# Kernel tuning notes

Measured on AMD Instinct MI355X. Metric: run time of the kernel, lower is better.

Reference implementation:

```python
import jax, jax.numpy as jnp
import numpy as np
from jax.scipy.special import logsumexp

B = 2048       # anchors
P = 4          # positives per anchor (constant -> ragged list collapses to [B,P])
D = 256        # embed dim
N_NEG = 32768  # shared negative bank
TEMPERATURE = 0.05
ALPHA = 0.1
EPS = 1e-12    # F.normalize eps


def _l2norm(x):
    n = jnp.sqrt(jnp.sum(x * x, axis=-1, keepdims=True))
    return x / jnp.maximum(n, EPS)


def setup_inputs() -> dict:
    key = jax.random.key(0)
    k1, k2, k3 = jax.random.split(key, 3)
    return {
        "anchor_embeddings": jax.random.normal(k1, (B, D), jnp.float32),
        "positive_embeddings": jax.random.normal(k2, (B * P, D), jnp.float32),
        "negative_embeddings": jax.random.normal(k3, (N_NEG, D), jnp.float32),
        "num_positives_per_anchor": jnp.full((B,), P, dtype=jnp.int32),
    }


def reference(anchor_embeddings, positive_embeddings, negative_embeddings,
              num_positives_per_anchor):
    a = _l2norm(anchor_embeddings)                       # [B, D]
    p = _l2norm(positive_embeddings).reshape(B, P, D)    # [B, P, D]
    n = _l2norm(negative_embeddings)                     # [N, D]

    pos_sim = jnp.einsum("bd,bpd->bp", a, p) / TEMPERATURE   # [B, P]
    neg_sim = jnp.einsum("bd,nd->bn", a, n) / TEMPERATURE    # [B, N]  (dominant traffic)
    neg_lse = logsumexp(neg_sim, axis=1)                     # [B]

    # per-(anchor, positive) CE with label 0 over logits [pos_j, neg_sim_i]:
    # loss = logsumexp([pos_j, neg...]) - pos_j = logaddexp(pos_j, neg_lse_i) - pos_j
    pair_loss = jnp.logaddexp(pos_sim, neg_lse[:, None]) - pos_sim   # [B, P]
    counts = num_positives_per_anchor
    pair_mask = jnp.arange(P)[None, :] < counts[:, None]             # [B, P]
    total = jnp.sum(jnp.where(pair_mask, pair_loss, 0.0))

    # weighted-positive term (only for anchors with num_pos > 1)
    w = jax.nn.softmax(pos_sim, axis=1)                  # [B, P]
    wps = jnp.sum(w * pos_sim, axis=1)                   # [B]
    wloss = jnp.logaddexp(wps, neg_lse) - wps            # [B]
    total = total + ALPHA * jnp.sum(jnp.where(counts > 1, wloss, 0.0))

    return total / B
```

## Files before the change

kernel.cpp:

```cpp
#include <hip/hip_runtime.h>
#include <math.h>

constexpr int   B       = 2048;
constexpr int   P       = 4;
constexpr int   D       = 256;
constexpr int   NNEG    = 32768;
constexpr int   NTILES  = NNEG / 64;
constexpr float TEMP    = 0.05f;
constexpr float ALPHA   = 0.1f;
constexpr float EPS     = 1e-12f;
constexpr float INV_T   = 1.0f / TEMP;
constexpr float SCALE_Q = 28.853900817779268f;

typedef __bf16 bf16x8 __attribute__((ext_vector_type(8)));
typedef float  f32x4  __attribute__((ext_vector_type(4)));

__device__ inline unsigned short f2bf(float f) {
  unsigned int u = __float_as_uint(f);
  u = (u + 0x7fffu + ((u >> 16) & 1u)) >> 16;
  return (unsigned short)u;
}


__global__ void prep_kernel(const float* __restrict__ a,
                            const float* __restrict__ pzx,
                            const float* __restrict__ n,
                            unsigned short* __restrict__ a_bf,
                            unsigned short* __restrict__ n_bf,
                            float* __restrict__ pos_sim,
                            float* __restrict__ loss_acc,
                            unsigned int* __restrict__ ticket) {
  if (blockIdx.x == 0 && threadIdx.x == 0) { *loss_acc = 0.0f; *ticket = 0u; }
  int w    = (blockIdx.x * blockDim.x + threadIdx.x) >> 6;
  int lane = threadIdx.x & 63;
  if (w < B + NNEG) {
    const float* src; unsigned short* dstm; int row; float post;
    if (w < B) { src = a + (size_t)w * D;       dstm = a_bf; row = w;     post = SCALE_Q; }
    else       { src = n + (size_t)(w - B) * D; dstm = n_bf; row = w - B; post = 1.0f; }
    float4 v = ((const float4*)src)[lane];
    float ss = v.x * v.x + v.y * v.y + v.z * v.z + v.w * v.w;
#pragma unroll
    for (int off = 32; off > 0; off >>= 1) ss += __shfl_xor(ss, off, 64);
    float inv = post / fmaxf(sqrtf(ss), EPS);
    ushort4 o;
    o.x = f2bf(v.x * inv); o.y = f2bf(v.y * inv);
    o.z = f2bf(v.z * inv); o.w = f2bf(v.w * inv);
    const int p = row >> 4, r = row & 15;
    const int c = lane >> 3, q = (lane >> 1) & 3, j0 = (lane & 1) * 4;
    *(ushort4*)(dstm + (size_t)p * 4096 + c * 512 + q * 128 + r * 8 + j0) = o;
  } else {
    int pw = w - (B + NNEG);
    if (pw >= B * P) return;
    int b = pw >> 2;
    float4 av = ((const float4*)(a + (size_t)b * D))[lane];
    float4 pv = ((const float4*)(pzx + (size_t)pw * D))[lane];
    float d  = av.x * pv.x + av.y * pv.y + av.z * pv.z + av.w * pv.w;
    float sa = av.x * av.x + av.y * av.y + av.z * av.z + av.w * av.w;
    float sp = pv.x * pv.x + pv.y * pv.y + pv.z * pv.z + pv.w * pv.w;
#pragma unroll
    for (int off = 32; off > 0; off >>= 1) {
      d  += __shfl_xor(d, off, 64);
      sa += __shfl_xor(sa, off, 64);
      sp += __shfl_xor(sp, off, 64);
    }
    if (lane == 0) {
      float inva = 1.0f / fmaxf(sqrtf(sa), EPS);
      float invp = 1.0f / fmaxf(sqrtf(sp), EPS);
      pos_sim[pw] = d * inva * invp * INV_T;
    }
  }
}

constexpr int BM = 64, BN = 256;

__global__ __launch_bounds__(256, 4) void negsim_mfma_kernel(
    const unsigned short* __restrict__ Af,
    const unsigned short* __restrict__ Nf,
    float* __restrict__ part_s) {
  __shared__ __align__(16) unsigned short As[32 * 512];

  const int tid  = threadIdx.x;
  const int wave = tid >> 6;
  const int lane = tid & 63;

  const int id   = blockIdx.x;
  const int xcd  = id & 7;
  const int j    = id >> 3;
  const int nblk = xcd * 16 + (j & 15);
  const int mblk = j >> 4;
  const int m0   = mblk * BM;
  const int n0   = nblk * BN;

#pragma unroll
  for (int t = 0; t < 8; t++) {
    const int f = wave * 8 + t;
    const int c = f >> 2, p = f & 3;
    __builtin_amdgcn_global_load_lds(
        (const __attribute__((address_space(1))) unsigned int*)
            (Af + (size_t)((m0 >> 4) + p) * 4096 + c * 512 + lane * 8),
        (__attribute__((address_space(3))) unsigned int*)(As + f * 512 + lane * 8),
        16, 0, 0);
  }
  __syncthreads();

  const unsigned short* Bp = Nf + (size_t)((n0 >> 4) + wave * 4) * 4096 + lane * 8;

  f32x4 acc[4][4] = {};
  bf16x8 b0[4], b1[4];

#pragma unroll
  for (int ni = 0; ni < 4; ni++)
    b0[ni] = *(const bf16x8*)(Bp + (size_t)ni * 4096);

#pragma unroll
  for (int c = 0; c < 8; c += 2) {
#pragma unroll
    for (int ni = 0; ni < 4; ni++)
      b1[ni] = *(const bf16x8*)(Bp + (size_t)ni * 4096 + (c + 1) * 512);
    {
      bf16x8 af[4];
#pragma unroll
      for (int mi = 0; mi < 4; mi++)
        af[mi] = *(const bf16x8*)&As[(c * 4 + mi) * 512 + lane * 8];
#pragma unroll
      for (int mi = 0; mi < 4; mi++)
#pragma unroll
        for (int ni = 0; ni < 4; ni++)
          acc[mi][ni] = __builtin_amdgcn_mfma_f32_16x16x32_bf16(
              af[mi], b0[ni], acc[mi][ni], 0, 0, 0);
    }
    if (c + 2 < 8) {
#pragma unroll
      for (int ni = 0; ni < 4; ni++)
        b0[ni] = *(const bf16x8*)(Bp + (size_t)ni * 4096 + (c + 2) * 512);
    }
    {
      bf16x8 af[4];
#pragma unroll
      for (int mi = 0; mi < 4; mi++)
        af[mi] = *(const bf16x8*)&As[((c + 1) * 4 + mi) * 512 + lane * 8];
#pragma unroll
      for (int mi = 0; mi < 4; mi++)
#pragma unroll
        for (int ni = 0; ni < 4; ni++)
          acc[mi][ni] = __builtin_amdgcn_mfma_f32_16x16x32_bf16(
              af[mi], b1[ni], acc[mi][ni], 0, 0, 0);
    }
  }

#pragma unroll
  for (int mi = 0; mi < 4; mi++) {
#pragma unroll
    for (int rr = 0; rr < 4; rr++) {
      float s = __builtin_amdgcn_exp2f(acc[mi][0][rr]) +
                __builtin_amdgcn_exp2f(acc[mi][1][rr]) +
                __builtin_amdgcn_exp2f(acc[mi][2][rr]) +
                __builtin_amdgcn_exp2f(acc[mi][3][rr]);
#pragma unroll
      for (int off = 1; off < 16; off <<= 1) s += __shfl_xor(s, off, 64);
      if ((lane & 15) == 0) {
        int row = m0 + mi * 16 + (lane >> 4) * 4 + rr;
        part_s[(size_t)row * NTILES + (nblk * 4 + wave)] = s;
      }
    }
  }
}

__global__ void loss_kernel(const float* __restrict__ part_s,
                            const float* __restrict__ pos_sim,
                            const int* __restrict__ counts,
                            float* __restrict__ loss_acc,
                            unsigned int* __restrict__ ticket,
                            float* __restrict__ out) {
  const int tid = threadIdx.x;
  const int b   = blockIdx.x * 16 + (tid >> 4);
  const int sub = tid & 15;
  const float* ps = part_s + (size_t)b * NTILES;
  float s = 0.0f;
#pragma unroll
  for (int i = 0; i < NTILES / 16; i++) s += ps[sub + i * 16];
  s += __shfl_xor(s, 1, 64);
  s += __shfl_xor(s, 2, 64);
  s += __shfl_xor(s, 4, 64);
  s += __shfl_xor(s, 8, 64);

  float acc = 0.0f;
  if (sub == 0) {
    float L = logf(s);
    float p0 = pos_sim[b * P + 0], p1 = pos_sim[b * P + 1];
    float p2 = pos_sim[b * P + 2], p3 = pos_sim[b * P + 3];
    int cnt = counts[b];
    float pj[P] = {p0, p1, p2, p3};
#pragma unroll
    for (int jj = 0; jj < P; jj++) {
      if (jj < cnt) {
        float hi = fmaxf(pj[jj], L), lo = fminf(pj[jj], L);
        acc += hi + log1pf(__expf(lo - hi)) - pj[jj];
      }
    }
    float mp = fmaxf(fmaxf(p0, p1), fmaxf(p2, p3));
    float e0 = __expf(p0 - mp), e1 = __expf(p1 - mp);
    float e2 = __expf(p2 - mp), e3 = __expf(p3 - mp);
    float se = e0 + e1 + e2 + e3;
    float wps = (e0 * p0 + e1 * p1 + e2 * p2 + e3 * p3) / se;
    if (cnt > 1) {
      float hi = fmaxf(wps, L), lo = fminf(wps, L);
      acc += ALPHA * (hi + log1pf(__expf(lo - hi)) - wps);
    }
  }
#pragma unroll
  for (int off = 32; off > 0; off >>= 1) acc += __shfl_xor(acc, off, 64);
  __shared__ float sa[4];
  int wid = tid >> 6, lane = tid & 63;
  if (lane == 0) sa[wid] = acc;
  __syncthreads();
  if (tid == 0) {
    atomicAdd(loss_acc, sa[0] + sa[1] + sa[2] + sa[3]);
    __threadfence();
    unsigned int t = atomicAdd(ticket, 1u);
    if (t == (unsigned int)gridDim.x - 1u) {
      float total = atomicAdd(loss_acc, 0.0f);
      out[0] = total / (float)B;
    }
  }
}

extern "C" void kernel_launch(void* const* d_in, const int* in_sizes, int n_in,
                              void* d_out, int out_size, void* d_ws,
                              size_t ws_size, hipStream_t stream) {
  const float* anc    = (const float*)d_in[0];
  const float* pos    = (const float*)d_in[1];
  const float* neg    = (const float*)d_in[2];
  const int*   counts = (const int*)d_in[3];
  float* out = (float*)d_out;

  unsigned short* a_bf = (unsigned short*)d_ws;
  unsigned short* n_bf = a_bf + (size_t)B * D;
  float* part_s  = (float*)(n_bf + (size_t)NNEG * D);
  float* pos_sim = part_s + (size_t)B * NTILES;
  float* loss_acc = pos_sim + B * P;
  unsigned int* ticket = (unsigned int*)(loss_acc + 1);

  prep_kernel<<<(B + NNEG + B * P) / 4, 256, 0, stream>>>(
      anc, pos, neg, a_bf, n_bf, pos_sim, loss_acc, ticket);

  negsim_mfma_kernel<<<4096, 256, 0, stream>>>(a_bf, n_bf, part_s);

  loss_kernel<<<B / 16, 256, 0, stream>>>(part_s, pos_sim, counts,
                                          loss_acc, ticket, out);
}
```

Baseline: 138.2 us.

## Switch negsim GEMM to 32x32x16 MFMA with matching 32-row packed layout

Replaces the 16x16x32 bf16 MFMA tiling (4x4 accumulators per wave) with 32x32x16 MFMAs (2x2 accumulators per wave) and repacks the bf16 anchor and negative buffers into 32-row blocks to match the new operand layout. The B operand is prefetched with a three-deep register ring over 16 k-steps instead of double buffering. Larger MFMA shapes reduce the number of instructions issued and the LDS/register operand traffic per FLOP. The epilogue row reduction now shuffles across 32 lanes instead of 16, which adds shuffle work.

After: 156.1 us. +13.0%, slower.

```diff
diff --git a/kernel.cpp b/kernel.cpp
--- a/kernel.cpp
+++ b/kernel.cpp
@@ -13,7 +13,7 @@
 constexpr float SCALE_Q = 28.853900817779268f;
 
 typedef __bf16 bf16x8 __attribute__((ext_vector_type(8)));
-typedef float  f32x4  __attribute__((ext_vector_type(4)));
+typedef float  f32x16 __attribute__((ext_vector_type(16)));
 
 __device__ inline unsigned short f2bf(float f) {
   unsigned int u = __float_as_uint(f);
@@ -45,9 +45,9 @@
     ushort4 o;
     o.x = f2bf(v.x * inv); o.y = f2bf(v.y * inv);
     o.z = f2bf(v.z * inv); o.w = f2bf(v.w * inv);
-    const int p = row >> 4, r = row & 15;
-    const int c = lane >> 3, q = (lane >> 1) & 3, j0 = (lane & 1) * 4;
-    *(ushort4*)(dstm + (size_t)p * 4096 + c * 512 + q * 128 + r * 8 + j0) = o;
+    const int p = row >> 5, r = row & 31;
+    const int c = lane >> 2, h = (lane >> 1) & 1, j0 = (lane & 1) * 4;
+    *(ushort4*)(dstm + (size_t)p * 8192 + c * 512 + h * 256 + r * 8 + j0) = o;
   } else {
     int pw = w - (B + NNEG);
     if (pw >= B * P) return;
@@ -94,72 +94,56 @@
 #pragma unroll
   for (int t = 0; t < 8; t++) {
     const int f = wave * 8 + t;
-    const int c = f >> 2, p = f & 3;
+    const int c = f >> 1, pi = f & 1;
     __builtin_amdgcn_global_load_lds(
         (const __attribute__((address_space(1))) unsigned int*)
-            (Af + (size_t)((m0 >> 4) + p) * 4096 + c * 512 + lane * 8),
+            (Af + (size_t)((m0 >> 5) + pi) * 8192 + c * 512 + lane * 8),
         (__attribute__((address_space(3))) unsigned int*)(As + f * 512 + lane * 8),
         16, 0, 0);
   }
   __syncthreads();
 
-  const unsigned short* Bp = Nf + (size_t)((n0 >> 4) + wave * 4) * 4096 + lane * 8;
-
-  f32x4 acc[4][4] = {};
-  bf16x8 b0[4], b1[4];
-
-#pragma unroll
-  for (int ni = 0; ni < 4; ni++)
-    b0[ni] = *(const bf16x8*)(Bp + (size_t)ni * 4096);
-
-#pragma unroll
-  for (int c = 0; c < 8; c += 2) {
-#pragma unroll
-    for (int ni = 0; ni < 4; ni++)
-      b1[ni] = *(const bf16x8*)(Bp + (size_t)ni * 4096 + (c + 1) * 512);
-    {
-      bf16x8 af[4];
-#pragma unroll
-      for (int mi = 0; mi < 4; mi++)
-        af[mi] = *(const bf16x8*)&As[(c * 4 + mi) * 512 + lane * 8];
-#pragma unroll
-      for (int mi = 0; mi < 4; mi++)
-#pragma unroll
-        for (int ni = 0; ni < 4; ni++)
-          acc[mi][ni] = __builtin_amdgcn_mfma_f32_16x16x32_bf16(
-              af[mi], b0[ni], acc[mi][ni], 0, 0, 0);
-    }
-    if (c + 2 < 8) {
-#pragma unroll
-      for (int ni = 0; ni < 4; ni++)
-        b0[ni] = *(const bf16x8*)(Bp + (size_t)ni * 4096 + (c + 2) * 512);
-    }
-    {
-      bf16x8 af[4];
-#pragma unroll
-      for (int mi = 0; mi < 4; mi++)
-        af[mi] = *(const bf16x8*)&As[((c + 1) * 4 + mi) * 512 + lane * 8];
-#pragma unroll
-      for (int mi = 0; mi < 4; mi++)
-#pragma unroll
-        for (int ni = 0; ni < 4; ni++)
-          acc[mi][ni] = __builtin_amdgcn_mfma_f32_16x16x32_bf16(
-              af[mi], b1[ni], acc[mi][ni], 0, 0, 0);
-    }
-  }
-
-#pragma unroll
-  for (int mi = 0; mi < 4; mi++) {
-#pragma unroll
-    for (int rr = 0; rr < 4; rr++) {
-      float s = __builtin_amdgcn_exp2f(acc[mi][0][rr]) +
-                __builtin_amdgcn_exp2f(acc[mi][1][rr]) +
-                __builtin_amdgcn_exp2f(acc[mi][2][rr]) +
-                __builtin_amdgcn_exp2f(acc[mi][3][rr]);
-#pragma unroll
-      for (int off = 1; off < 16; off <<= 1) s += __shfl_xor(s, off, 64);
-      if ((lane & 15) == 0) {
-        int row = m0 + mi * 16 + (lane >> 4) * 4 + rr;
+  const unsigned short* Bp = Nf + (size_t)((n0 >> 5) + wave * 2) * 8192 + lane * 8;
+
+  f32x16 acc[2][2] = {};
+  bf16x8 bb[3][2];
+
+#pragma unroll
+  for (int ni = 0; ni < 2; ni++) {
+    bb[0][ni] = *(const bf16x8*)(Bp + (size_t)ni * 8192 + 0 * 512);
+    bb[1][ni] = *(const bf16x8*)(Bp + (size_t)ni * 8192 + 1 * 512);
+  }
+
+#pragma unroll
+  for (int c = 0; c < 16; c++) {
+    if (c + 2 < 16) {
+#pragma unroll
+      for (int ni = 0; ni < 2; ni++)
+        bb[(c + 2) % 3][ni] =
+            *(const bf16x8*)(Bp + (size_t)ni * 8192 + (c + 2) * 512);
+    }
+    bf16x8 af[2];
+#pragma unroll
+    for (int mi = 0; mi < 2; mi++)
+      af[mi] = *(const bf16x8*)&As[(c * 2 + mi) * 512 + lane * 8];
+#pragma unroll
+    for (int mi = 0; mi < 2; mi++)
+#pragma unroll
+      for (int ni = 0; ni < 2; ni++)
+        acc[mi][ni] = __builtin_amdgcn_mfma_f32_32x32x16_bf16(
+            af[mi], bb[c % 3][ni], acc[mi][ni], 0, 0, 0);
+  }
+
+#pragma unroll
+  for (int mi = 0; mi < 2; mi++) {
+#pragma unroll
+    for (int reg = 0; reg < 16; reg++) {
+      float s = __builtin_amdgcn_exp2f(acc[mi][0][reg]) +
+                __builtin_amdgcn_exp2f(acc[mi][1][reg]);
+#pragma unroll
+      for (int off = 1; off < 32; off <<= 1) s += __shfl_xor(s, off, 64);
+      if ((lane & 31) == 0) {
+        int row = m0 + mi * 32 + (reg & 3) + 8 * (reg >> 2) + 4 * (lane >> 5);
         part_s[(size_t)row * NTILES + (nblk * 4 + wave)] = s;
       }
     }
```
